# Kernel optimization log

Measured on AMD Instinct MI355X. Metric: run time of the kernel, lower is better.

The kernel has to match this reference:

```python
import jax, jax.numpy as jnp
import numpy as np

PRIMES = (1, 2654435761, 805459861, 3674653429)
N_PTS = 400000


def _flat_index(c, res, T, tiled):
    # c: [N, D] uint32 integer grid coords; returns int32 table indices in [0, T).
    Tm = jnp.uint32(T - 1)  # T is a power of two
    prod = int(np.prod(np.asarray(res, dtype=np.int64)))
    if tiled or prod <= T:
        strides = np.cumprod([1] + list(res[:-1])).astype(np.uint32)
        idx = jnp.sum(c * jnp.asarray(strides), axis=1)
    else:
        ps = jnp.asarray(np.array(PRIMES[: c.shape[1]], dtype=np.uint32))
        terms = c * ps
        idx = terms[:, 0]
        for d in range(1, c.shape[1]):
            idx = idx ^ terms[:, d]
    return (idx & Tm).astype(jnp.int32)


def grid_encode(x, table, base, growth, tiled=False, nearest=False):
    # x: [N, D] in [0,1); table: [L, T, F] -> [N, L*F]
    N, D = x.shape
    L, T, F = table.shape
    outs = []
    for l in range(L):
        res = [int(np.ceil(b * g ** l)) for b, g in zip(base, growth)]
        res_f = jnp.asarray(np.array(res, np.float32))
        pos = x * (res_f - 1.0)  # [N, D]
        if nearest:
            c = jnp.clip(jnp.rint(pos), 0.0, res_f - 1.0).astype(jnp.uint32)
            feat = table[l][_flat_index(c, res, T, tiled)]
        else:
            p0 = jnp.floor(pos)
            w = pos - p0  # trilinear weights, [N, D]
            feat = jnp.zeros((N, F), table.dtype)
            for corner in range(1 << D):
                offs = np.array([(corner >> d) & 1 for d in range(D)], np.float32)
                c = jnp.minimum(p0 + offs, res_f - 1.0).astype(jnp.uint32)
                wt = jnp.prod(jnp.where(offs > 0, w, 1.0 - w), axis=1, keepdims=True)
                feat = feat + wt * table[l][_flat_index(c, res, T, tiled)]
        outs.append(feat)
    return jnp.concatenate(outs, axis=1)


def setup_inputs() -> dict:
    key = jax.random.key(0)
    kx, ks, kt, km = jax.random.split(key, 4)
    x = jax.random.uniform(kx, (N_PTS, 4), dtype=jnp.float32)
    table_s = jax.random.normal(ks, (16, 1 << 19, 2), dtype=jnp.float32) * 0.1
    table_t = jax.random.normal(kt, (16, 1 << 19, 2), dtype=jnp.float32) * 0.1
    table_m = jax.random.normal(km, (1, 1 << 21, 1), dtype=jnp.float32) * 0.1
    return {"x": x, "table_s": table_s, "table_t": table_t, "table_m": table_m}


def reference(x, table_s, table_t, table_m):
    s_base, s_g = (16, 16, 16), (1.2, 1.2, 1.2)
    t_base, t_g = (16, 16, 16, 16), (1.2, 1.2, 1.2, 1.2)
    m_base, m_g = (128, 128, 128), (1.0, 1.0, 1.0)
    s = grid_encode(x[:, :3], table_s, s_base, s_g)                       # [N, 32]
    t = grid_encode(x, table_t, t_base, t_g)                              # [N, 32]
    m = jax.nn.sigmoid(grid_encode(x[:, :3], table_m, m_base, m_g, tiled=True, nearest=True))  # [N, 1]
    return s + t * (1.0 - m)
```

## Files before the change

### kernel.cpp

```cpp
#include <hip/hip_runtime.h>
#include <cstdint>

#define NLEV 16
#define TMASK ((1u << 19) - 1u)

typedef float f4v __attribute__((ext_vector_type(4)));
typedef float f2v __attribute__((ext_vector_type(2)));
typedef uint32_t u2v __attribute__((ext_vector_type(2)));

__constant__ int c_res[NLEV] = {16, 20, 24, 28, 34, 40, 48, 58, 69, 83,
                                100, 119, 143, 172, 206, 247};

__device__ __forceinline__ float bf_lo(uint32_t e) { return __uint_as_float(e << 16); }
__device__ __forceinline__ float bf_hi(uint32_t e) { return __uint_as_float(e & 0xFFFF0000u); }
__device__ __forceinline__ uint32_t rne16(float f) {
    uint32_t u = __float_as_uint(f);
    return (u + 0x7fffu + ((u >> 16) & 1u)) >> 16;
}

__global__ __launch_bounds__(256) void conv_kernel(
    const f4v* __restrict__ src_s, const f4v* __restrict__ src_t,
    u2v* __restrict__ dst_s, u2v* __restrict__ dst_t, int half)
{
    int i = blockIdx.x * 256 + threadIdx.x;
    const f4v* src = (i < half) ? src_s : src_t;
    u2v* dst = (i < half) ? dst_s : dst_t;
    int j = (i < half) ? i : i - half;
    if (j < half) {
        f4v v = __builtin_nontemporal_load(src + j);
        u2v o;
        o.x = rne16(v.x) | (rne16(v.y) << 16);
        o.y = rne16(v.z) | (rne16(v.w) << 16);
        __builtin_nontemporal_store(o, dst + j);
    }
}

__global__ __launch_bounds__(256) void m_kernel(
    const float* __restrict__ x, const float* __restrict__ tab_m,
    float* __restrict__ one_m, int N)
{
    int n = blockIdx.x * 256 + threadIdx.x;
    if (n >= N) return;
    f4v xv = __builtin_nontemporal_load((const f4v*)x + n);
    float q0 = fminf(fmaxf(rintf(xv.x * 127.0f), 0.0f), 127.0f);
    float q1 = fminf(fmaxf(rintf(xv.y * 127.0f), 0.0f), 127.0f);
    float q2 = fminf(fmaxf(rintf(xv.z * 127.0f), 0.0f), 127.0f);
    uint32_t idx = (uint32_t)q0 + ((uint32_t)q1 << 7) + ((uint32_t)q2 << 14);
    float v = tab_m[idx];
    float m = 1.0f / (1.0f + expf(-v));
    __builtin_nontemporal_store(1.0f - m, one_m + n);
}

template<bool IS_T>
__global__ __launch_bounds__(256, 4) void enc_kernel(
    const float* __restrict__ x,
    const uint32_t* __restrict__ tab,
    const float* __restrict__ one_m,
    f2v* __restrict__ ws, int N, int half_grid)
{
    const int NP = IS_T ? 8 : 4;

    int blk = blockIdx.x;
    int hi = (blk >= half_grid) ? 1 : 0;
    int blkp = blk - hi * half_grid;
    int l = (blkp & 7) + hi * 8;
    int n0 = ((blkp >> 3) << 9) + threadIdx.x;
    if (n0 >= N) return;
    int n1 = n0 + 256;
    bool has1 = (n1 < N);

    int r = c_res[l];
    uint32_t ru = (uint32_t)r;
    float rf1 = (float)r - 1.0f;
    const bool direct = IS_T ? (l <= 2) : (l <= 8);
    const uint32_t* tl = tab + ((size_t)l << 19);

    f4v xv[2];
    xv[0] = __builtin_nontemporal_load((const f4v*)x + n0);
    xv[1] = has1 ? __builtin_nontemporal_load((const f4v*)x + n1) : xv[0];

    float w0[2], w1[2], w2[2], w3[2];
    float fv1[2], fv2[2], fv3[2];
    uint32_t c0a[2];
    #pragma unroll
    for (int q = 0; q < 2; ++q) {
        float p0 = xv[q].x * rf1, p1 = xv[q].y * rf1, p2 = xv[q].z * rf1;
        float f0 = floorf(p0), f1 = floorf(p1), f2 = floorf(p2);
        w0[q] = p0 - f0; w1[q] = p1 - f1; w2[q] = p2 - f2;
        c0a[q] = (uint32_t)f0;
        fv1[q] = f1; fv2[q] = f2;
        if (IS_T) {
            float p3 = xv[q].w * rf1;
            float f3 = floorf(p3);
            w3[q] = p3 - f3; fv3[q] = f3;
        } else {
            w3[q] = 0.0f; fv3[q] = 0.0f;
        }
    }

    u2v pv[2][8];
    uint32_t ov[2][8];
    uint32_t swb[2], nb[2];
    #pragma unroll
    for (int q = 0; q < 2; ++q) {
        uint32_t sw = 0u, nd = 0u;
        #pragma unroll
        for (int pi = 0; pi < NP; ++pi) {
            float o1 = (float)(pi & 1);
            float o2 = (float)((pi >> 1) & 1);
            uint32_t c1 = (uint32_t)fminf(fv1[q] + o1, rf1);
            uint32_t c2 = (uint32_t)fminf(fv2[q] + o2, rf1);
            uint32_t ia, ib, needi;
            if (direct) {
                uint32_t base;
                if (IS_T) {
                    float o3 = (float)((pi >> 2) & 1);
                    uint32_t c3 = (uint32_t)fminf(fv3[q] + o3, rf1);
                    base = ru * (c1 + ru * (c2 + ru * c3));
                } else {
                    base = ru * (c1 + ru * c2);
                }
                ia = base + c0a[q];
                ib = ia + 1;
                needi = ia & 1u;
            } else {
                uint32_t hh = (c1 * 2654435761u) ^ (c2 * 805459861u);
                if (IS_T) {
                    float o3 = (float)((pi >> 2) & 1);
                    uint32_t c3 = (uint32_t)fminf(fv3[q] + o3, rf1);
                    hh ^= c3 * 3674653429u;
                }
                ia = (c0a[q] ^ hh) & TMASK;
                ib = ((c0a[q] + 1u) ^ hh) & TMASK;
                needi = c0a[q] & 1u;
            }
            pv[q][pi] = *(const u2v*)(tl + (ia & ~1u));
            if (needi) ov[q][pi] = tl[ib];
            sw |= (ia & 1u) << pi;
            nd |= needi << pi;
        }
        swb[q] = sw; nb[q] = nd;
    }

    f2v prevv[2];
    float omv[2];
    if (IS_T) {
        omv[0] = __builtin_nontemporal_load(one_m + n0);
        if (has1) omv[1] = __builtin_nontemporal_load(one_m + n1);
    } else {
        prevv[0] = __builtin_nontemporal_load(ws + (size_t)l * N + n0);
        if (has1) prevv[1] = __builtin_nontemporal_load(ws + (size_t)l * N + n1);
    }

    #pragma unroll
    for (int q = 0; q < 2; ++q) {
        float a0 = 0.0f, a1 = 0.0f;
        float wva = 1.0f - w0[q], wvb = w0[q];
        #pragma unroll
        for (int pi = 0; pi < NP; ++pi) {
            float bw = ((pi & 1) ? w1[q] : 1.0f - w1[q])
                     * (((pi >> 1) & 1) ? w2[q] : 1.0f - w2[q]);
            if (IS_T) bw *= (((pi >> 2) & 1) ? w3[q] : 1.0f - w3[q]);
            uint32_t sw = (swb[q] >> pi) & 1u;
            uint32_t ea = sw ? pv[q][pi].y : pv[q][pi].x;
            uint32_t eb = sw ? pv[q][pi].x : pv[q][pi].y;
            if ((nb[q] >> pi) & 1u) eb = ov[q][pi];
            float wa = bw * wva, wb = bw * wvb;
            a0 += wa * bf_lo(ea) + wb * bf_lo(eb);
            a1 += wa * bf_hi(ea) + wb * bf_hi(eb);
        }
        int n = q ? n1 : n0;
        bool ok = q ? has1 : true;
        if (ok) {
            if (IS_T) {
                f2v outv; outv.x = a0 * omv[q]; outv.y = a1 * omv[q];
                __builtin_nontemporal_store(outv, ws + (size_t)l * N + n);
            } else {
                f2v outv; outv.x = prevv[q].x + a0; outv.y = prevv[q].y + a1;
                __builtin_nontemporal_store(outv, ws + (size_t)l * N + n);
            }
        }
    }
}

__global__ __launch_bounds__(256) void out_kernel(
    const f2v* __restrict__ ws, f4v* __restrict__ out4, int N)
{
    __shared__ float lds[256 * 33];
    int tid = threadIdx.x;
    int n = (blockIdx.x << 8) + tid;

    if (n < N) {
        #pragma unroll
        for (int l = 0; l < NLEV; ++l) {
            f2v v = __builtin_nontemporal_load(ws + (size_t)l * N + n);
            lds[tid * 33 + 2 * l]     = v.x;
            lds[tid * 33 + 2 * l + 1] = v.y;
        }
    }
    __syncthreads();

    size_t out4base = (size_t)blockIdx.x * 2048;
    size_t limit = (size_t)N * 8;
    #pragma unroll
    for (int k = 0; k < 8; ++k) {
        int g = k * 256 + tid;
        size_t G = out4base + g;
        if (G < limit) {
            int p = g >> 3;
            int e = (g & 7) * 4;
            f4v v;
            v.x = lds[p * 33 + e];
            v.y = lds[p * 33 + e + 1];
            v.z = lds[p * 33 + e + 2];
            v.w = lds[p * 33 + e + 3];
            __builtin_nontemporal_store(v, out4 + G);
        }
    }
}

__global__ __launch_bounds__(256) void grid_enc_kernel(
    const float* __restrict__ x,
    const float* __restrict__ tab_s,
    const float* __restrict__ tab_t,
    const float* __restrict__ tab_m,
    float* __restrict__ out, int N)
{
    int tid = blockIdx.x * blockDim.x + threadIdx.x;
    if (tid >= N * NLEV) return;
    int n = tid >> 4, l = tid & 15;
    float x0 = x[n*4+0], x1 = x[n*4+1], x2 = x[n*4+2], x3 = x[n*4+3];
    float one_m;
    {
        float q0 = fminf(fmaxf(rintf(x0*127.0f),0.0f),127.0f);
        float q1 = fminf(fmaxf(rintf(x1*127.0f),0.0f),127.0f);
        float q2 = fminf(fmaxf(rintf(x2*127.0f),0.0f),127.0f);
        uint32_t idx = (uint32_t)q0 + ((uint32_t)q1<<7) + ((uint32_t)q2<<14);
        one_m = 1.0f - 1.0f/(1.0f + expf(-tab_m[idx]));
    }
    int r = c_res[l]; uint32_t ru = (uint32_t)r; float rf1 = (float)r - 1.0f;
    float p0 = x0*rf1, p1 = x1*rf1, p2 = x2*rf1, p3 = x3*rf1;
    float f0 = floorf(p0), f1 = floorf(p1), f2 = floorf(p2), f3 = floorf(p3);
    float w0 = p0-f0, w1 = p1-f1, w2 = p2-f2, w3 = p3-f3;
    const float2* ts2 = (const float2*)tab_s + ((size_t)l<<19);
    const float2* tt2 = (const float2*)tab_t + ((size_t)l<<19);
    const bool sd = (l<=8), td = (l<=2);
    float s0=0,s1=0;
    #pragma unroll
    for (int c = 0; c < 8; ++c) {
        uint32_t c0 = (uint32_t)fminf(f0+(float)(c&1), rf1);
        uint32_t c1 = (uint32_t)fminf(f1+(float)((c>>1)&1), rf1);
        uint32_t c2 = (uint32_t)fminf(f2+(float)((c>>2)&1), rf1);
        float wt = ((c&1)?w0:1.0f-w0)*(((c>>1)&1)?w1:1.0f-w1)*(((c>>2)&1)?w2:1.0f-w2);
        uint32_t idx = sd ? (c0 + c1*ru + c2*ru*ru)
                          : (c0 ^ (c1*2654435761u) ^ (c2*805459861u));
        float2 e = ts2[idx & TMASK]; s0 += wt*e.x; s1 += wt*e.y;
    }
    float t0=0,t1=0;
    #pragma unroll
    for (int c = 0; c < 16; ++c) {
        uint32_t c0 = (uint32_t)fminf(f0+(float)(c&1), rf1);
        uint32_t c1 = (uint32_t)fminf(f1+(float)((c>>1)&1), rf1);
        uint32_t c2 = (uint32_t)fminf(f2+(float)((c>>2)&1), rf1);
        uint32_t c3 = (uint32_t)fminf(f3+(float)((c>>3)&1), rf1);
        float wt = ((c&1)?w0:1.0f-w0)*(((c>>1)&1)?w1:1.0f-w1)
                 *(((c>>2)&1)?w2:1.0f-w2)*(((c>>3)&1)?w3:1.0f-w3);
        uint32_t idx = td ? (c0 + ru*(c1 + ru*(c2 + ru*c3)))
                          : (c0 ^ (c1*2654435761u) ^ (c2*805459861u) ^ (c3*3674653429u));
        float2 e = tt2[idx & TMASK]; t0 += wt*e.x; t1 += wt*e.y;
    }
    size_t o = (size_t)n*32 + 2*(size_t)l;
    out[o] = s0 + t0*one_m; out[o+1] = s1 + t1*one_m;
}

extern "C" void kernel_launch(void* const* d_in, const int* in_sizes, int n_in,
                              void* d_out, int out_size, void* d_ws, size_t ws_size,
                              hipStream_t stream) {
    const float* x     = (const float*)d_in[0];
    const float* tab_s = (const float*)d_in[1];
    const float* tab_t = (const float*)d_in[2];
    const float* tab_m = (const float*)d_in[3];
    float* out = (float*)d_out;

    int N = in_sizes[0] / 4;
    size_t wm_b = (((size_t)N * 4) + 255) & ~(size_t)255;
    size_t wc_b = (size_t)N * NLEV * 8;
    size_t tb_b = (size_t)NLEV * (1u << 19) * 4;
    int nchunk = (N + 255) / 256;
    int nch2 = (N + 511) / 512;

    if (ws_size >= wm_b + wc_b + 2 * tb_b) {
        float* wm = (float*)d_ws;
        f2v*   wc = (f2v*)((char*)d_ws + wm_b);
        uint32_t* ps = (uint32_t*)((char*)d_ws + wm_b + wc_b);
        uint32_t* pt = ps + (size_t)NLEV * (1u << 19);
        int half = NLEV * (1 << 19) / 2;
        int half_grid = 8 * nch2;
        conv_kernel<<<(2 * half + 255) / 256, 256, 0, stream>>>(
            (const f4v*)tab_s, (const f4v*)tab_t, (u2v*)ps, (u2v*)pt, half);
        m_kernel<<<nchunk, 256, 0, stream>>>(x, tab_m, wm, N);
        enc_kernel<true><<<16 * nch2, 256, 0, stream>>>(x, pt, wm, wc, N, half_grid);
        enc_kernel<false><<<16 * nch2, 256, 0, stream>>>(x, ps, wm, wc, N, half_grid);
        out_kernel<<<nchunk, 256, 0, stream>>>(wc, (f4v*)out, N);
    } else {
        int total = N * NLEV;
        grid_enc_kernel<<<(total + 255) / 256, 256, 0, stream>>>(x, tab_s, tab_t, tab_m, out, N);
    }
}
```

Measured before the change: 616.8 us.

## Fuse spatial and temporal hash-grid encode kernels into one pass

Merges the two templated encode launches (4D temporal, then 3D spatial) into a single kernel that gathers from both tables for the same level and point. It then writes s + t*(1-m) directly, which removes one kernel launch, the intermediate write of the t result and its re-read by the spatial pass, and the duplicate x loads and weight computation. The cost is more live registers per thread (12 corners times 2 points of gathered pairs), which under launch_bounds(256,4) may cause spills or lower occupancy.

```diff
diff --git a/kernel.cpp b/kernel.cpp
--- a/kernel.cpp
+++ b/kernel.cpp
@@ -51,15 +51,13 @@
     __builtin_nontemporal_store(1.0f - m, one_m + n);
 }
 
-template<bool IS_T>
-__global__ __launch_bounds__(256, 4) void enc_kernel(
+__global__ __launch_bounds__(256, 4) void enc_fused(
     const float* __restrict__ x,
-    const uint32_t* __restrict__ tab,
+    const uint32_t* __restrict__ tabS,
+    const uint32_t* __restrict__ tabT,
     const float* __restrict__ one_m,
     f2v* __restrict__ ws, int N, int half_grid)
 {
-    const int NP = IS_T ? 8 : 4;
-
     int blk = blockIdx.x;
     int hi = (blk >= half_grid) ? 1 : 0;
     int blkp = blk - hi * half_grid;
@@ -72,8 +70,9 @@
     int r = c_res[l];
     uint32_t ru = (uint32_t)r;
     float rf1 = (float)r - 1.0f;
-    const bool direct = IS_T ? (l <= 2) : (l <= 8);
-    const uint32_t* tl = tab + ((size_t)l << 19);
+    const bool dirS = (l <= 8), dirT = (l <= 2);
+    const uint32_t* tlS = tabS + ((size_t)l << 19);
+    const uint32_t* tlT = tabT + ((size_t)l << 19);
 
     f4v xv[2];
     xv[0] = __builtin_nontemporal_load((const f4v*)x + n0);
@@ -89,96 +88,119 @@
         w0[q] = p0 - f0; w1[q] = p1 - f1; w2[q] = p2 - f2;
         c0a[q] = (uint32_t)f0;
         fv1[q] = f1; fv2[q] = f2;
-        if (IS_T) {
-            float p3 = xv[q].w * rf1;
-            float f3 = floorf(p3);
-            w3[q] = p3 - f3; fv3[q] = f3;
-        } else {
-            w3[q] = 0.0f; fv3[q] = 0.0f;
-        }
-    }
-
-    u2v pv[2][8];
-    uint32_t ov[2][8];
-    uint32_t swb[2], nb[2];
+        float p3 = xv[q].w * rf1;
+        float f3 = floorf(p3);
+        w3[q] = p3 - f3; fv3[q] = f3;
+    }
+
+    u2v pvT[2][8];
+    uint32_t ovT[2][8];
+    uint32_t swT[2], nbT[2];
     #pragma unroll
     for (int q = 0; q < 2; ++q) {
         uint32_t sw = 0u, nd = 0u;
         #pragma unroll
-        for (int pi = 0; pi < NP; ++pi) {
+        for (int pi = 0; pi < 8; ++pi) {
+            float o1 = (float)(pi & 1);
+            float o2 = (float)((pi >> 1) & 1);
+            float o3 = (float)((pi >> 2) & 1);
+            uint32_t c1 = (uint32_t)fminf(fv1[q] + o1, rf1);
+            uint32_t c2 = (uint32_t)fminf(fv2[q] + o2, rf1);
+            uint32_t c3 = (uint32_t)fminf(fv3[q] + o3, rf1);
+            uint32_t ia, ib, needi;
+            if (dirT) {
+                uint32_t base = ru * (c1 + ru * (c2 + ru * c3));
+                ia = base + c0a[q];
+                ib = ia + 1;
+                needi = ia & 1u;
+            } else {
+                uint32_t hh = (c1 * 2654435761u) ^ (c2 * 805459861u)
+                            ^ (c3 * 3674653429u);
+                ia = (c0a[q] ^ hh) & TMASK;
+                ib = ((c0a[q] + 1u) ^ hh) & TMASK;
+                needi = c0a[q] & 1u;
+            }
+            pvT[q][pi] = *(const u2v*)(tlT + (ia & ~1u));
+            if (needi) ovT[q][pi] = tlT[ib];
+            sw |= (ia & 1u) << pi;
+            nd |= needi << pi;
+        }
+        swT[q] = sw; nbT[q] = nd;
+    }
+
+    u2v pvS[2][4];
+    uint32_t ovS[2][4];
+    uint32_t swS[2], nbS[2];
+    #pragma unroll
+    for (int q = 0; q < 2; ++q) {
+        uint32_t sw = 0u, nd = 0u;
+        #pragma unroll
+        for (int pi = 0; pi < 4; ++pi) {
             float o1 = (float)(pi & 1);
             float o2 = (float)((pi >> 1) & 1);
             uint32_t c1 = (uint32_t)fminf(fv1[q] + o1, rf1);
             uint32_t c2 = (uint32_t)fminf(fv2[q] + o2, rf1);
             uint32_t ia, ib, needi;
-            if (direct) {
-                uint32_t base;
-                if (IS_T) {
-                    float o3 = (float)((pi >> 2) & 1);
-                    uint32_t c3 = (uint32_t)fminf(fv3[q] + o3, rf1);
-                    base = ru * (c1 + ru * (c2 + ru * c3));
-                } else {
-                    base = ru * (c1 + ru * c2);
-                }
+            if (dirS) {
+                uint32_t base = ru * (c1 + ru * c2);
                 ia = base + c0a[q];
                 ib = ia + 1;
                 needi = ia & 1u;
             } else {
                 uint32_t hh = (c1 * 2654435761u) ^ (c2 * 805459861u);
-                if (IS_T) {
-                    float o3 = (float)((pi >> 2) & 1);
-                    uint32_t c3 = (uint32_t)fminf(fv3[q] + o3, rf1);
-                    hh ^= c3 * 3674653429u;
-                }
                 ia = (c0a[q] ^ hh) & TMASK;
                 ib = ((c0a[q] + 1u) ^ hh) & TMASK;
                 needi = c0a[q] & 1u;
             }
-            pv[q][pi] = *(const u2v*)(tl + (ia & ~1u));
-            if (needi) ov[q][pi] = tl[ib];
+            pvS[q][pi] = *(const u2v*)(tlS + (ia & ~1u));
+            if (needi) ovS[q][pi] = tlS[ib];
             sw |= (ia & 1u) << pi;
             nd |= needi << pi;
         }
-        swb[q] = sw; nb[q] = nd;
-    }
-
-    f2v prevv[2];
+        swS[q] = sw; nbS[q] = nd;
+    }
+
     float omv[2];
-    if (IS_T) {
-        omv[0] = __builtin_nontemporal_load(one_m + n0);
-        if (has1) omv[1] = __builtin_nontemporal_load(one_m + n1);
-    } else {
-        prevv[0] = __builtin_nontemporal_load(ws + (size_t)l * N + n0);
-        if (has1) prevv[1] = __builtin_nontemporal_load(ws + (size_t)l * N + n1);
-    }
+    omv[0] = __builtin_nontemporal_load(one_m + n0);
+    omv[1] = has1 ? __builtin_nontemporal_load(one_m + n1) : 0.0f;
 
     #pragma unroll
     for (int q = 0; q < 2; ++q) {
-        float a0 = 0.0f, a1 = 0.0f;
+        float t0 = 0.0f, t1 = 0.0f;
         float wva = 1.0f - w0[q], wvb = w0[q];
         #pragma unroll
-        for (int pi = 0; pi < NP; ++pi) {
+        for (int pi = 0; pi < 8; ++pi) {
+            float bw = ((pi & 1) ? w1[q] : 1.0f - w1[q])
+                     * (((pi >> 1) & 1) ? w2[q] : 1.0f - w2[q])
+                     * (((pi >> 2) & 1) ? w3[q] : 1.0f - w3[q]);
+            uint32_t sw = (swT[q] >> pi) & 1u;
+            uint32_t ea = sw ? pvT[q][pi].y : pvT[q][pi].x;
+            uint32_t eb = sw ? pvT[q][pi].x : pvT[q][pi].y;
+            if ((nbT[q] >> pi) & 1u) eb = ovT[q][pi];
+            float wa = bw * wva, wb = bw * wvb;
+            t0 += wa * bf_lo(ea) + wb * bf_lo(eb);
+            t1 += wa * bf_hi(ea) + wb * bf_hi(eb);
+        }
+        float s0 = 0.0f, s1 = 0.0f;
+        #pragma unroll
+        for (int pi = 0; pi < 4; ++pi) {
             float bw = ((pi & 1) ? w1[q] : 1.0f - w1[q])
                      * (((pi >> 1) & 1) ? w2[q] : 1.0f - w2[q]);
-            if (IS_T) bw *= (((pi >> 2) & 1) ? w3[q] : 1.0f - w3[q]);
-            uint32_t sw = (swb[q] >> pi) & 1u;
-            uint32_t ea = sw ? pv[q][pi].y : pv[q][pi].x;
-            uint32_t eb = sw ? pv[q][pi].x : pv[q][pi].y;
-            if ((nb[q] >> pi) & 1u) eb = ov[q][pi];
+            uint32_t sw = (swS[q] >> pi) & 1u;
+            uint32_t ea = sw ? pvS[q][pi].y : pvS[q][pi].x;
+            uint32_t eb = sw ? pvS[q][pi].x : pvS[q][pi].y;
+            if ((nbS[q] >> pi) & 1u) eb = ovS[q][pi];
             float wa = bw * wva, wb = bw * wvb;
-            a0 += wa * bf_lo(ea) + wb * bf_lo(eb);
-            a1 += wa * bf_hi(ea) + wb * bf_hi(eb);
-        }
-        int n = q ? n1 : n0;
+            s0 += wa * bf_lo(ea) + wb * bf_lo(eb);
+            s1 += wa * bf_hi(ea) + wb * bf_hi(eb);
+        }
         bool ok = q ? has1 : true;
         if (ok) {
-            if (IS_T) {
-                f2v outv; outv.x = a0 * omv[q]; outv.y = a1 * omv[q];
-                __builtin_nontemporal_store(outv, ws + (size_t)l * N + n);
-            } else {
-                f2v outv; outv.x = prevv[q].x + a0; outv.y = prevv[q].y + a1;
-                __builtin_nontemporal_store(outv, ws + (size_t)l * N + n);
-            }
+            int n = q ? n1 : n0;
+            f2v outv;
+            outv.x = s0 + t0 * omv[q];
+            outv.y = s1 + t1 * omv[q];
+            __builtin_nontemporal_store(outv, ws + (size_t)l * N + n);
         }
     }
 }
@@ -299,8 +321,7 @@
         conv_kernel<<<(2 * half + 255) / 256, 256, 0, stream>>>(
             (const f4v*)tab_s, (const f4v*)tab_t, (u2v*)ps, (u2v*)pt, half);
         m_kernel<<<nchunk, 256, 0, stream>>>(x, tab_m, wm, N);
-        enc_kernel<true><<<16 * nch2, 256, 0, stream>>>(x, pt, wm, wc, N, half_grid);
-        enc_kernel<false><<<16 * nch2, 256, 0, stream>>>(x, ps, wm, wc, N, half_grid);
+        enc_fused<<<16 * nch2, 256, 0, stream>>>(x, ps, pt, wm, wc, N, half_grid);
         out_kernel<<<nchunk, 256, 0, stream>>>(wc, (f4v*)out, N);
     } else {
         int total = N * NLEV;
```

After: 658.2 us. +6.7%, slower.
